# Kernel optimization log

Hardware: AMD Instinct MI355X
Metric: run time of the kernel (lower is better)

Reference implementation:

```python
import jax, jax.numpy as jnp
import numpy as np

HIDDEN = 2304
HEADS = 16
THETA = 10000.0
LN_EPS = 1e-5


def setup_inputs() -> dict:
    key = jax.random.key(0)
    ks = jax.random.split(key, 6)
    d = HIDDEN
    init = lambda k, shape: jax.random.normal(k, shape, jnp.float32) * 0.02
    return {
        "x": jax.random.normal(ks[0], (4, 2048, d), jnp.float32),
        "wq": init(ks[1], (d, d)), "bq": jnp.zeros((d,), jnp.float32),
        "wk": init(ks[2], (d, d)), "bk": jnp.zeros((d,), jnp.float32),
        "wv": init(ks[3], (d, d)), "bv": jnp.zeros((d,), jnp.float32),
        "wo": init(ks[4], (d, d)), "bo": jnp.zeros((d,), jnp.float32),
        "ln_g": jnp.ones((d,), jnp.float32),
        "ln_b": jnp.zeros((d,), jnp.float32),
    }


def reference(x, wq, bq, wk, bk, wv, bv, wo, bo, ln_g, ln_b):
    b, s, d = x.shape
    H = HEADS
    Dh = d // H

    # qkv projections (nn.Linear: x @ W^T + b)
    q = jnp.einsum('bsd,ed->bse', x, wq) + bq
    k = jnp.einsum('bsd,ed->bse', x, wk) + bk
    v = jnp.einsum('bsd,ed->bse', x, wv) + bv

    # RoPE over the FULL hidden dim (d/2 pairs), as in the source
    pos = jnp.arange(s, dtype=jnp.float32)                    # (s,)
    scale = jnp.arange(0, d, 2, dtype=jnp.float32) / d        # (d/2,)
    omega = 1.0 / (THETA ** scale)                            # (d/2,)
    ang = pos[:, None] * omega[None, :]                       # (s, d/2)
    cos, sin = jnp.cos(ang), jnp.sin(ang)

    def rot(t):
        t2 = t.reshape(b, s, d // 2, 2)
        x0, x1 = t2[..., 0], t2[..., 1]
        return jnp.stack([cos * x0 - sin * x1, sin * x0 + cos * x1], axis=-1).reshape(b, s, d)

    q, k = rot(q), rot(k)

    # split heads -> (b, H, s, Dh)
    q = q.reshape(b, s, H, Dh).transpose(0, 2, 1, 3)
    k = k.reshape(b, s, H, Dh).transpose(0, 2, 1, 3)
    v = v.reshape(b, s, H, Dh).transpose(0, 2, 1, 3)

    # NOTE: faithful to source: einsum labels make this HEAD-mixing
    # attention at each position: logits shape (b, H, s, H)
    att_scale = 1.0 / (Dh ** 0.5)
    logits = jnp.einsum('bnhd,bmhd->bnhm', q, k) * att_scale
    w = jax.nn.softmax(logits, axis=-1)                       # (b,H,s,H)
    out = jnp.einsum('bnhm,bmhd->bnhd', w, v)                 # (b,H,s,Dh)

    out = out.transpose(0, 2, 1, 3).reshape(b, s, d)
    out = jnp.einsum('bsd,ed->bse', out, wo) + bo

    # residual + LayerNorm (dropout in eval mode -> identity)
    y = x + out
    mu = jnp.mean(y, axis=-1, keepdims=True)
    var = jnp.mean((y - mu) ** 2, axis=-1, keepdims=True)
    return (y - mu) * jax.lax.rsqrt(var + LN_EPS) * ln_g + ln_b
```

## Files before the change

### kernel.cpp

```cpp
#include <hip/hip_runtime.h>
#include <stdint.h>
#include <stddef.h>

#define D_HID 2304
#define NTOK  8192
#define NQKV  6912
#define WELEMS 5308416
#define SEQ_MASK 2047

typedef unsigned short u16;
typedef __bf16 bf16x8 __attribute__((ext_vector_type(8)));
typedef float  f32x16 __attribute__((ext_vector_type(16)));

__device__ __forceinline__ u16 f2bf(float f) {
    unsigned int u = __builtin_bit_cast(unsigned int, f);
    u += 0x7fffu + ((u >> 16) & 1u);
    return (u16)(u >> 16);
}
__device__ __forceinline__ float bf2f(u16 h) {
    unsigned int u = ((unsigned int)h) << 16;
    return __builtin_bit_cast(float, u);
}

__device__ __forceinline__ void gl2lds16(const void* g, void* l) {
    __builtin_amdgcn_global_load_lds(
        (const __attribute__((address_space(1))) void*)g,
        (__attribute__((address_space(3))) void*)l,
        16, 0, 0);
}

__global__ __launch_bounds__(256) void cvt_f32_bf16(
    const float* __restrict__ src, u16* __restrict__ dst)
{
    size_t i = ((size_t)blockIdx.x * 256 + threadIdx.x) * 4;
    float4 f = *(const float4*)(src + i);
    ushort4 o = make_ushort4(f2bf(f.x), f2bf(f.y), f2bf(f.z), f2bf(f.w));
    *(ushort4*)(dst + i) = o;
}

__global__ __launch_bounds__(256) void cvt_weights(
    const float* __restrict__ wq, const float* __restrict__ wk,
    const float* __restrict__ wv, const float* __restrict__ wo,
    u16* __restrict__ dst,
    const float* __restrict__ bq, const float* __restrict__ bk,
    const float* __restrict__ bv, float* __restrict__ bqkv)
{
    int i = blockIdx.x * 256 + threadIdx.x;
    if (i < NQKV)
        bqkv[i] = (i < 2304) ? bq[i] : (i < 4608) ? bk[i - 2304] : bv[i - 4608];
    size_t base = (size_t)i * 4;
    int r = (int)(base / WELEMS);
    const float* src = (r == 0) ? wq : (r == 1) ? wk : (r == 2) ? wv : wo;
    float4 f = *(const float4*)(src + (base - (size_t)r * WELEMS));
    ushort4 o = make_ushort4(f2bf(f.x), f2bf(f.y), f2bf(f.z), f2bf(f.w));
    *(ushort4*)(dst + base) = o;
}

template<int MODE>
__global__ __launch_bounds__(256, 3) void gemm_bt(
    const u16* __restrict__ A, const u16* __restrict__ B,
    const float* __restrict__ bias, u16* __restrict__ Cout,
    const float* __restrict__ resid, int M, int N, int K)
{
    __shared__ __align__(16) u16 As[128 * 64];
    __shared__ __align__(16) u16 Bs[128 * 64];

    const int tid  = threadIdx.x;
    const int lane = tid & 63;
    const int wave = tid >> 6;
    const int bm = blockIdx.y, bn = blockIdx.x;

    const int srow = tid >> 3;
    const int sc   = (tid & 7) ^ (srow & 7);
    const u16* Ag = A + (size_t)(bm * 128 + srow) * K + sc * 8;
    const u16* Bg = B + (size_t)(bn * 128 + srow) * K + sc * 8;
    const size_t row32 = (size_t)32 * K;
    u16* asd = As + wave * 512;
    u16* bsd = Bs + wave * 512;

    const int rl = lane & 31;
    const int h  = lane >> 5;
    const int swz = rl & 7;
    const int wm = (wave >> 1) * 64;
    const int wn = (wave & 1) * 64;

    f32x16 acc[2][2] = {};

    for (int kb = 0; kb < K; kb += 64) {
        __syncthreads();
#pragma unroll
        for (int r = 0; r < 4; ++r) {
            gl2lds16(Ag + kb + r * row32, asd + r * 2048);
            gl2lds16(Bg + kb + r * row32, bsd + r * 2048);
        }
        __syncthreads();

#pragma unroll
        for (int s = 0; s < 4; ++s) {
            const int ch = ((s * 2 + h) ^ swz) * 8;
            bf16x8 a0 = *(const bf16x8*)(As + (wm      + rl) * 64 + ch);
            bf16x8 a1 = *(const bf16x8*)(As + (wm + 32 + rl) * 64 + ch);
            bf16x8 b0 = *(const bf16x8*)(Bs + (wn      + rl) * 64 + ch);
            bf16x8 b1 = *(const bf16x8*)(Bs + (wn + 32 + rl) * 64 + ch);
            acc[0][0] = __builtin_amdgcn_mfma_f32_32x32x16_bf16(a0, b0, acc[0][0], 0, 0, 0);
            acc[0][1] = __builtin_amdgcn_mfma_f32_32x32x16_bf16(a0, b1, acc[0][1], 0, 0, 0);
            acc[1][0] = __builtin_amdgcn_mfma_f32_32x32x16_bf16(a1, b0, acc[1][0], 0, 0, 0);
            acc[1][1] = __builtin_amdgcn_mfma_f32_32x32x16_bf16(a1, b1, acc[1][1], 0, 0, 0);
        }
    }

#pragma unroll
    for (int mt = 0; mt < 2; ++mt) {
#pragma unroll
        for (int nt = 0; nt < 2; ++nt) {
            const int gn = bn * 128 + wn + nt * 32 + rl;
            const float bv = bias[gn];
#pragma unroll
            for (int reg = 0; reg < 16; ++reg) {
                const int gm = bm * 128 + wm + mt * 32 +
                               (reg & 3) + 8 * (reg >> 2) + 4 * h;
                const size_t idx = (size_t)gm * N + gn;
                float v = acc[mt][nt][reg] + bv;
                if constexpr (MODE == 1) v += resid[idx];
                Cout[idx] = f2bf(v);
            }
        }
    }
}

__global__ __launch_bounds__(256) void attn_headmix(
    const u16* __restrict__ QKV, u16* __restrict__ Aout)
{
    __shared__ __align__(16) float qs[D_HID];
    __shared__ __align__(16) float ks[D_HID];
    __shared__ __align__(16) float vs[D_HID];
    __shared__ float wsm[256];

    const int tid = threadIdx.x;
    const int t   = blockIdx.x;
    const float fpos = (float)(t & SEQ_MASK);
    const u16* row = QKV + (size_t)t * NQKV;

    const float OMEGA_C = -2.0f * 13.287712379549449f / 2304.0f;
    const float INV2PI  = 0.15915494309189535f;

    for (int c = tid; c < 864; c += 256) {
        uint4 raw = *(const uint4*)(row + c * 8);
        float f[8];
        f[0] = bf2f(raw.x & 0xffff); f[1] = bf2f(raw.x >> 16);
        f[2] = bf2f(raw.y & 0xffff); f[3] = bf2f(raw.y >> 16);
        f[4] = bf2f(raw.z & 0xffff); f[5] = bf2f(raw.z >> 16);
        f[6] = bf2f(raw.w & 0xffff); f[7] = bf2f(raw.w >> 16);
        if (c < 576) {
            const int cc = (c < 288) ? c : c - 288;
            const int p0 = cc * 4;
#pragma unroll
            for (int jp = 0; jp < 4; ++jp) {
                float omega = exp2f((float)(p0 + jp) * OMEGA_C);
                float rr = fpos * omega * INV2PI;
                rr -= floorf(rr);
                float sn = __builtin_amdgcn_sinf(rr);
                float cs = __builtin_amdgcn_cosf(rr);
                float x0 = f[2 * jp], x1 = f[2 * jp + 1];
                f[2 * jp]     = cs * x0 - sn * x1;
                f[2 * jp + 1] = sn * x0 + cs * x1;
            }
            float* dst = ((c < 288) ? qs : ks) + cc * 8;
            *(float4*)(dst)     = make_float4(f[0], f[1], f[2], f[3]);
            *(float4*)(dst + 4) = make_float4(f[4], f[5], f[6], f[7]);
        } else {
            float* dst = vs + (c - 576) * 8;
            *(float4*)(dst)     = make_float4(f[0], f[1], f[2], f[3]);
            *(float4*)(dst + 4) = make_float4(f[4], f[5], f[6], f[7]);
        }
    }
    __syncthreads();

    const int n = tid >> 4, m = tid & 15;
    const float* qr = qs + n * 144;
    const float* kr = ks + m * 144;
    float s = 0.f;
#pragma unroll
    for (int d = 0; d < 144; d += 4) {
        float4 qv = *(const float4*)(qr + d);
        float4 kv = *(const float4*)(kr + d);
        s += qv.x * kv.x + qv.y * kv.y + qv.z * kv.z + qv.w * kv.w;
    }
    s *= (1.0f / 12.0f);

    float mx = s;
#pragma unroll
    for (int off = 8; off >= 1; off >>= 1) mx = fmaxf(mx, __shfl_xor(mx, off));
    float e = __expf(s - mx);
    float sum = e;
#pragma unroll
    for (int off = 8; off >= 1; off >>= 1) sum += __shfl_xor(sum, off);
    wsm[tid] = e / sum;
    __syncthreads();

    u16* orow = Aout + (size_t)t * D_HID;
#pragma unroll
    for (int r = 0; r < 9; ++r) {
        int o  = tid + r * 256;
        int on = o / 144;
        int od = o - on * 144;
        const float* wrow = wsm + on * 16;
        const float* vcol = vs + od;
        float a = 0.f;
#pragma unroll
        for (int mm = 0; mm < 16; ++mm) a += wrow[mm] * vcol[mm * 144];
        orow[o] = f2bf(a);
    }
}

__global__ __launch_bounds__(256) void ln_kernel(
    const u16* __restrict__ Y, const float* __restrict__ g,
    const float* __restrict__ b, float* __restrict__ out)
{
    const int tid  = threadIdx.x;
    const u16* y = Y + (size_t)blockIdx.x * D_HID;
    float v[9];
    float s = 0.f, s2 = 0.f;
#pragma unroll
    for (int r = 0; r < 9; ++r) {
        v[r] = bf2f(y[tid + r * 256]);
        s += v[r]; s2 += v[r] * v[r];
    }
#pragma unroll
    for (int off = 32; off >= 1; off >>= 1) {
        s  += __shfl_xor(s, off);
        s2 += __shfl_xor(s2, off);
    }
    __shared__ float red[8];
    const int wave = tid >> 6;
    if ((tid & 63) == 0) { red[wave] = s; red[4 + wave] = s2; }
    __syncthreads();
    s  = red[0] + red[1] + red[2] + red[3];
    s2 = red[4] + red[5] + red[6] + red[7];
    const float inv_n = 1.0f / 2304.0f;
    float mu  = s * inv_n;
    float var = fmaxf(s2 * inv_n - mu * mu, 0.f);
    float inv = rsqrtf(var + 1e-5f);
    float* orow = out + (size_t)blockIdx.x * D_HID;
#pragma unroll
    for (int r = 0; r < 9; ++r) {
        int c = tid + r * 256;
        orow[c] = (v[r] - mu) * inv * g[c] + b[c];
    }
}

extern "C" void kernel_launch(void* const* d_in, const int* in_sizes, int n_in,
                              void* d_out, int out_size, void* d_ws, size_t ws_size,
                              hipStream_t stream)
{
    const float* x   = (const float*)d_in[0];
    const float* wq  = (const float*)d_in[1];
    const float* bq  = (const float*)d_in[2];
    const float* wk  = (const float*)d_in[3];
    const float* bk  = (const float*)d_in[4];
    const float* wv  = (const float*)d_in[5];
    const float* bv  = (const float*)d_in[6];
    const float* wo  = (const float*)d_in[7];
    const float* bo  = (const float*)d_in[8];
    const float* lng = (const float*)d_in[9];
    const float* lnb = (const float*)d_in[10];

    char* ws = (char*)d_ws;
    size_t off = 0;
    auto alloc = [&](size_t bytes) {
        void* p = ws + off;
        off += (bytes + 255) & ~(size_t)255;
        return p;
    };
    u16*   xb   = (u16*)alloc((size_t)NTOK * D_HID * 2);
    u16*   wqkv = (u16*)alloc((size_t)(NQKV + D_HID) * D_HID * 2);
    u16*   wob  = wqkv + (size_t)NQKV * D_HID;
    float* bqkv = (float*)alloc((size_t)NQKV * 4);
    u16*   qkv  = (u16*)alloc((size_t)NTOK * NQKV * 2);
    u16*   aout = (u16*)alloc((size_t)NTOK * D_HID * 2);
    u16*   ybuf = qkv;

    cvt_f32_bf16<<<NTOK * D_HID / 1024, 256, 0, stream>>>(x, xb);
    cvt_weights<<<4 * WELEMS / 1024, 256, 0, stream>>>(wq, wk, wv, wo, wqkv,
                                                       bq, bk, bv, bqkv);
    gemm_bt<0><<<dim3(NQKV / 128, NTOK / 128), 256, 0, stream>>>(
        xb, wqkv, bqkv, qkv, nullptr, NTOK, NQKV, D_HID);
    attn_headmix<<<NTOK, 256, 0, stream>>>(qkv, aout);
    gemm_bt<1><<<dim3(D_HID / 128, NTOK / 128), 256, 0, stream>>>(
        aout, wob, bo, ybuf, x, NTOK, D_HID, D_HID);
    ln_kernel<<<NTOK, 256, 0, stream>>>(ybuf, lng, lnb, (float*)d_out);
}
```

Baseline: 746.0 us.

## Swizzle GEMM block order, pad attention LDS rows, vectorize head-mix output, bf16 residual

The GEMMs now take a 1D grid and remap block indices into groups of 8 M-tiles per N column, so neighbouring blocks share A and B tiles in L2. The attention kernel pads per-head LDS rows to 148 floats to cut bank conflicts. Its weighted-V stage is rewritten so 144 threads each compute a 4x4 register tile and store with vector writes. The output-projection residual now reads the bf16 copy of x instead of fp32, halving that traffic but adding rounding error to the residual.

```diff
diff --git a/kernel.cpp b/kernel.cpp
--- a/kernel.cpp
+++ b/kernel.cpp
@@ -60,7 +60,7 @@
 __global__ __launch_bounds__(256, 3) void gemm_bt(
     const u16* __restrict__ A, const u16* __restrict__ B,
     const float* __restrict__ bias, u16* __restrict__ Cout,
-    const float* __restrict__ resid, int M, int N, int K)
+    const u16* __restrict__ resid, int M, int N, int K)
 {
     __shared__ __align__(16) u16 As[128 * 64];
     __shared__ __align__(16) u16 Bs[128 * 64];
@@ -68,7 +68,11 @@
     const int tid  = threadIdx.x;
     const int lane = tid & 63;
     const int wave = tid >> 6;
-    const int bm = blockIdx.y, bn = blockIdx.x;
+
+    const int num_bn = N >> 7;
+    const int rem = blockIdx.x % (num_bn << 3);
+    const int bn  = rem >> 3;
+    const int bm  = ((blockIdx.x / (num_bn << 3)) << 3) + (rem & 7);
 
     const int srow = tid >> 3;
     const int sc   = (tid & 7) ^ (srow & 7);
@@ -121,20 +125,21 @@
                                (reg & 3) + 8 * (reg >> 2) + 4 * h;
                 const size_t idx = (size_t)gm * N + gn;
                 float v = acc[mt][nt][reg] + bv;
-                if constexpr (MODE == 1) v += resid[idx];
+                if constexpr (MODE == 1) v += bf2f(resid[idx]);
                 Cout[idx] = f2bf(v);
             }
         }
     }
 }
 
+#define HROW 148
 __global__ __launch_bounds__(256) void attn_headmix(
     const u16* __restrict__ QKV, u16* __restrict__ Aout)
 {
-    __shared__ __align__(16) float qs[D_HID];
-    __shared__ __align__(16) float ks[D_HID];
-    __shared__ __align__(16) float vs[D_HID];
-    __shared__ float wsm[256];
+    __shared__ __align__(16) float qs[16 * HROW];
+    __shared__ __align__(16) float ks[16 * HROW];
+    __shared__ __align__(16) float vs[16 * HROW];
+    __shared__ __align__(16) float wsmT[256];
 
     const int tid = threadIdx.x;
     const int t   = blockIdx.x;
@@ -165,11 +170,14 @@
                 f[2 * jp]     = cs * x0 - sn * x1;
                 f[2 * jp + 1] = sn * x0 + cs * x1;
             }
-            float* dst = ((c < 288) ? qs : ks) + cc * 8;
+            const int hr = cc / 18, col = (cc - hr * 18) * 8;
+            float* dst = ((c < 288) ? qs : ks) + hr * HROW + col;
             *(float4*)(dst)     = make_float4(f[0], f[1], f[2], f[3]);
             *(float4*)(dst + 4) = make_float4(f[4], f[5], f[6], f[7]);
         } else {
-            float* dst = vs + (c - 576) * 8;
+            const int cv = c - 576;
+            const int hr = cv / 18, col = (cv - hr * 18) * 8;
+            float* dst = vs + hr * HROW + col;
             *(float4*)(dst)     = make_float4(f[0], f[1], f[2], f[3]);
             *(float4*)(dst + 4) = make_float4(f[4], f[5], f[6], f[7]);
         }
@@ -177,8 +185,8 @@
     __syncthreads();
 
     const int n = tid >> 4, m = tid & 15;
-    const float* qr = qs + n * 144;
-    const float* kr = ks + m * 144;
+    const float* qr = qs + n * HROW;
+    const float* kr = ks + m * HROW;
     float s = 0.f;
 #pragma unroll
     for (int d = 0; d < 144; d += 4) {
@@ -195,21 +203,32 @@
     float sum = e;
 #pragma unroll
     for (int off = 8; off >= 1; off >>= 1) sum += __shfl_xor(sum, off);
-    wsm[tid] = e / sum;
+    wsmT[m * 16 + n] = e / sum;
     __syncthreads();
 
-    u16* orow = Aout + (size_t)t * D_HID;
-#pragma unroll
-    for (int r = 0; r < 9; ++r) {
-        int o  = tid + r * 256;
-        int on = o / 144;
-        int od = o - on * 144;
-        const float* wrow = wsm + on * 16;
-        const float* vcol = vs + od;
-        float a = 0.f;
-#pragma unroll
-        for (int mm = 0; mm < 16; ++mm) a += wrow[mm] * vcol[mm * 144];
-        orow[o] = f2bf(a);
+    if (tid < 144) {
+        const int col4 = tid % 36;
+        const int nq   = tid / 36;
+        const int oc   = col4 * 4;
+        float4 a0 = {0,0,0,0}, a1 = {0,0,0,0}, a2 = {0,0,0,0}, a3 = {0,0,0,0};
+#pragma unroll
+        for (int mm = 0; mm < 16; ++mm) {
+            float4 w4 = *(const float4*)(wsmT + mm * 16 + nq * 4);
+            float4 v4 = *(const float4*)(vs + mm * HROW + oc);
+            a0.x += w4.x * v4.x; a0.y += w4.x * v4.y; a0.z += w4.x * v4.z; a0.w += w4.x * v4.w;
+            a1.x += w4.y * v4.x; a1.y += w4.y * v4.y; a1.z += w4.y * v4.z; a1.w += w4.y * v4.w;
+            a2.x += w4.z * v4.x; a2.y += w4.z * v4.y; a2.z += w4.z * v4.z; a2.w += w4.z * v4.w;
+            a3.x += w4.w * v4.x; a3.y += w4.w * v4.y; a3.z += w4.w * v4.z; a3.w += w4.w * v4.w;
+        }
+        u16* orow = Aout + (size_t)t * D_HID;
+        float4 accs[4] = {a0, a1, a2, a3};
+#pragma unroll
+        for (int i = 0; i < 4; ++i) {
+            const int nn = nq * 4 + i;
+            ushort4 o = make_ushort4(f2bf(accs[i].x), f2bf(accs[i].y),
+                                     f2bf(accs[i].z), f2bf(accs[i].w));
+            *(ushort4*)(orow + nn * 144 + oc) = o;
+        }
     }
 }
 
@@ -283,10 +302,10 @@
     cvt_f32_bf16<<<NTOK * D_HID / 1024, 256, 0, stream>>>(x, xb);
     cvt_weights<<<4 * WELEMS / 1024, 256, 0, stream>>>(wq, wk, wv, wo, wqkv,
                                                        bq, bk, bv, bqkv);
-    gemm_bt<0><<<dim3(NQKV / 128, NTOK / 128), 256, 0, stream>>>(
+    gemm_bt<0><<<(NQKV / 128) * (NTOK / 128), 256, 0, stream>>>(
         xb, wqkv, bqkv, qkv, nullptr, NTOK, NQKV, D_HID);
     attn_headmix<<<NTOK, 256, 0, stream>>>(qkv, aout);
-    gemm_bt<1><<<dim3(D_HID / 128, NTOK / 128), 256, 0, stream>>>(
-        aout, wob, bo, ybuf, x, NTOK, D_HID, D_HID);
+    gemm_bt<1><<<(D_HID / 128) * (NTOK / 128), 256, 0, stream>>>(
+        aout, wob, bo, ybuf, xb, NTOK, D_HID, D_HID);
     ln_kernel<<<NTOK, 256, 0, stream>>>(ybuf, lng, lnb, (float*)d_out);
 }
```

After: 694.3 us. 1.07x faster.
